# Optimization experiments

Hardware: AMD Instinct MI355X
Metric: run time of the kernel (lower is better)

The kernel has to match this reference:

```python
import jax, jax.numpy as jnp
import numpy as np

B = 16384    # batch of game states
HAND = 8     # max_hand_size
A = 30       # max_actions
C = 4        # max cards per action combo
E = 32       # card_embed_dim
HID = 128    # hidden_dim


def _encode_cards(cards, val_emb, suit_emb, type_emb):
    # cards: int array, 0 = padding, 53 = joker (treated as padding for value/suit)
    invalid = (cards == 0) | (cards == 53)
    values = jnp.where(invalid, 0, (cards - 1) % 13 + 1)
    suits = jnp.where(invalid, 0, (cards - 1) // 13 + 1)
    ce = jnp.concatenate([val_emb[values], suit_emb[suits]], axis=-1)  # [..., E]
    ct = jnp.where(values == 11, 1, jnp.where(values == 12, 2, jnp.where(values == 13, 3, 0)))
    te = type_emb[ct]  # [..., 8]
    pad = jnp.zeros(te.shape[:-1] + (E - te.shape[-1],), ce.dtype)
    return ce + jnp.concatenate([te, pad], axis=-1)


def _mha(q, kv, wq, bq, wk, bk, wv, bv, wo, bo, nh, kpm=None):
    b, sq, e = q.shape
    sk = kv.shape[1]
    hd = e // nh
    Q = (q @ wq + bq).reshape(b, sq, nh, hd)
    K = (kv @ wk + bk).reshape(b, sk, nh, hd)
    V = (kv @ wv + bv).reshape(b, sk, nh, hd)
    s = jnp.einsum('bqhd,bkhd->bhqk', Q, K) * (1.0 / np.sqrt(hd))
    if kpm is not None:  # kpm True = valid key
        s = s + jnp.where(kpm[:, None, None, :], 0.0, -1e9)
    a = jax.nn.softmax(s, axis=-1)
    o = jnp.einsum('bhqk,bkhd->bqhd', a, V).reshape(b, sq, e)
    return o @ wo + bo


def _combo_features(cards):
    # cards: [A, C] int, 0 = padding. Vectorized version of _compute_combo_features.
    mask = cards != 0
    combo_size = mask.sum(1).astype(jnp.float32)
    values = jnp.where(mask, (cards - 1) % 13 + 1, 0)
    has_valid = mask.any(1)
    fidx = jnp.argmax(mask, axis=1)
    fv = values[jnp.arange(cards.shape[0]), fidx]  # first valid value per action
    same = jnp.where(mask, values == fv[:, None], True).all(1).astype(jnp.float32)
    vf = values.astype(jnp.float32)
    attack = jnp.where(values == 1, 1.0,
             jnp.where(values == 11, 10.0,
             jnp.where(values == 12, 15.0,
             jnp.where(values == 13, 20.0, vf))))
    total = (attack * mask).sum(1)
    suits = jnp.where(mask, (cards - 1) // 13 + 1, 0)
    uniq = jnp.stack([(suits == s).any(1) for s in (1, 2, 3, 4)], 0).sum(0).astype(jnp.float32)
    ace = ((values == 1) & mask).any(1).astype(jnp.float32)
    valid = ((combo_size <= 4.0) & ((same > 0) | (ace > 0))).astype(jnp.float32)
    feats = jnp.stack([combo_size, same, total, uniq, ace, valid], axis=1)  # [A, 6]
    return jnp.where(has_valid[:, None], feats, 0.0), has_valid


def _forward(hand_cards, enemy_card, hand_size, game_state, discard_pile_cards,
             action_card_indices, num_valid_actions,
             val_emb, suit_emb, type_emb,
             ce_w1, ce_b1, ce_w2, ce_b2,
             ha_wq, ha_bq, ha_wk, ha_bk, ha_wv, ha_bv, ha_wo, ha_bo,
             he_wq, he_bq, he_wk, he_bk, he_wv, he_bv, he_wo, he_bo,
             se_w1, se_b1, se_w2, se_b2,
             atc_w1, atc_b1, atc_w2, atc_b2,
             as_w1, as_b1, as_w2, as_b2, as_w3, as_b3,
             cx_w1, cx_b1, cx_w2, cx_b2, cx_w3, cx_b3):
    relu = jax.nn.relu
    hand_emb = _encode_cards(hand_cards, val_emb, suit_emb, type_emb)            # [B, HAND, E]
    enemy_emb = _encode_cards(enemy_card[:, None], val_emb, suit_emb, type_emb)  # [B, 1, E]
    hand_mask = hand_cards != 0
    attended = _mha(hand_emb, hand_emb, ha_wq, ha_bq, ha_wk, ha_bk, ha_wv, ha_bv, ha_wo, ha_bo, 8, kpm=hand_mask)
    ctx_he = _mha(attended, enemy_emb, he_wq, he_bq, he_wk, he_bk, he_wv, he_bv, he_wo, he_bo, 4)
    lengths = jnp.maximum(hand_size.astype(jnp.float32), 1.0)[:, None]
    hand_ctx = ctx_he.sum(1) / lengths                                           # [B, E]

    # strategic features (batched per game state)
    hvals = jnp.where(hand_cards == 0, 0, (hand_cards - 1) % 13 + 1)
    hsz = hand_size.astype(jnp.float32)
    aces = (hvals == 1).sum(1).astype(jnp.float32)
    faces = ((hvals >= 11) & (hvals <= 13)).sum(1).astype(jnp.float32)
    low = ((hvals >= 2) & (hvals <= 6)).sum(1).astype(jnp.float32)
    hsuits = jnp.where(hand_cards == 0, 0, (hand_cards - 1) // 13 + 1)
    scnt = [(hsuits == s).sum(1).astype(jnp.float32) for s in (1, 2, 3, 4)]
    hvr = faces / (hsz + 1e-8)
    sdiv = jnp.stack([(hsuits == s).any(1) for s in (1, 2, 3, 4)], 0).sum(0).astype(jnp.float32) / 4.0
    strat = jnp.stack([hsz, aces, faces, low, scnt[0], scnt[1], scnt[2], scnt[3], hvr, sdiv], axis=1)
    strat_in = jnp.concatenate([game_state, strat], axis=1)                      # [B, 20]
    strat_ctx = relu(strat_in @ se_w1 + se_b1) @ se_w2 + se_b2                   # [B, 32]

    combined = jnp.concatenate([hand_ctx, enemy_emb[:, 0], strat_ctx, discard_pile_cards], axis=1)  # [B, 150]
    h = relu(combined @ cx_w1 + cx_b1)
    h = relu(h @ cx_w2 + cx_b2)
    ctx = h @ cx_w3 + cx_b3                                                      # [B, HID]
    type_probs = jax.nn.softmax(relu(ctx @ atc_w1 + atc_b1) @ atc_w2 + atc_b2, axis=-1)  # [B, 4]

    feats, has_valid = _combo_features(action_card_indices)                      # [A, 6], [A]
    emb = _encode_cards(action_card_indices, val_emb, suit_emb, type_emb)        # [A, C, E]
    m = (action_card_indices != 0).astype(emb.dtype)[..., None]
    cnt = jnp.maximum(m.sum(1), 1.0)
    act_emb = (emb * m).sum(1) / cnt                                             # masked mean over real cards
    act_emb = jnp.where(has_valid[:, None], act_emb, 0.0)
    combo_enc = relu(feats @ ce_w1 + ce_b1) @ ce_w2 + ce_b2                      # [A, 16]

    Bn = ctx.shape[0]
    af = jnp.concatenate([
        jnp.broadcast_to(ctx[:, None, :], (Bn, A, HID)),
        jnp.broadcast_to(act_emb[None], (Bn, A, E)),
        jnp.broadcast_to(combo_enc[None], (Bn, A, 16)),
    ], axis=-1)                                                                  # [B, A, 176]
    s = relu(af @ as_w1 + as_b1)
    s = relu(s @ as_w2 + as_b2)
    score = (s @ as_w3 + as_b3)[..., 0]                                          # [B, A]

    strength = feats[:, 2] / 20.0                                                # [A]
    bonus_valid = type_probs[:, 0:1] * strength[None, :] + type_probs[:, 1:2] * (1.0 - strength[None, :])
    bonus_empty = jnp.broadcast_to(type_probs[:, 3:4] * 2.0, (Bn, A))
    bonus = jnp.where(has_valid[None, :], bonus_valid, bonus_empty)
    return score + bonus                                                          # [B, A]


def setup_inputs() -> dict:
    key = jax.random.key(0)
    ki = iter(jax.random.split(key, 64))
    def nrm(shape, s):
        return (s * jax.random.normal(next(ki), shape)).astype(jnp.float32)
    def lin(i, o, s=0.08):
        return nrm((i, o), s), nrm((o,), 0.02)
    d = {}
    hc = jax.random.randint(next(ki), (B, HAND), 0, 53)
    d['hand_cards'] = hc.at[:, 0].set(jax.random.randint(next(ki), (B,), 1, 53))  # at least one valid card per hand
    d['enemy_card'] = jax.random.randint(next(ki), (B,), 1, 53)
    d['hand_size'] = jax.random.randint(next(ki), (B,), 1, 9)
    d['game_state'] = nrm((B, 10), 1.0)
    d['discard_pile_cards'] = jax.random.uniform(next(ki), (B, 54), dtype=jnp.float32)
    d['action_card_indices'] = jax.random.randint(next(ki), (A, C), 1, 53)
    d['num_valid_actions'] = A
    d['val_emb'] = nrm((14, 16), 0.1).at[0].set(0.0)   # padding_idx=0
    d['suit_emb'] = nrm((5, 16), 0.1).at[0].set(0.0)   # padding_idx=0
    d['type_emb'] = nrm((4, 8), 0.1)
    d['ce_w1'], d['ce_b1'] = lin(6, 32)
    d['ce_w2'], d['ce_b2'] = lin(32, 16)
    for p in ('ha', 'he'):
        for t in ('q', 'k', 'v', 'o'):
            d[p + '_w' + t], d[p + '_b' + t] = lin(E, E)
    d['se_w1'], d['se_b1'] = lin(20, 64)
    d['se_w2'], d['se_b2'] = lin(64, 32)
    d['atc_w1'], d['atc_b1'] = lin(HID, 64)
    d['atc_w2'], d['atc_b2'] = lin(64, 4)
    d['as_w1'], d['as_b1'] = lin(HID + E + 16, 64)
    d['as_w2'], d['as_b2'] = lin(64, 32)
    d['as_w3'], d['as_b3'] = lin(32, 1)
    d['cx_w1'], d['cx_b1'] = lin(2 * E + 32 + 54, HID)
    d['cx_w2'], d['cx_b2'] = lin(HID, HID)
    d['cx_w3'], d['cx_b3'] = lin(HID, HID)
    return d


def reference(hand_cards, enemy_card, hand_size, game_state, discard_pile_cards,
              action_card_indices, num_valid_actions,
              val_emb, suit_emb, type_emb,
              ce_w1, ce_b1, ce_w2, ce_b2,
              ha_wq, ha_bq, ha_wk, ha_bk, ha_wv, ha_bv, ha_wo, ha_bo,
              he_wq, he_bq, he_wk, he_bk, he_wv, he_bv, he_wo, he_bo,
              se_w1, se_b1, se_w2, se_b2,
              atc_w1, atc_b1, atc_w2, atc_b2,
              as_w1, as_b1, as_w2, as_b2, as_w3, as_b3,
              cx_w1, cx_b1, cx_w2, cx_b2, cx_w3, cx_b3):
    return _forward(hand_cards, enemy_card, hand_size, game_state, discard_pile_cards,
                    action_card_indices, num_valid_actions,
                    val_emb, suit_emb, type_emb,
                    ce_w1, ce_b1, ce_w2, ce_b2,
                    ha_wq, ha_bq, ha_wk, ha_bk, ha_wv, ha_bv, ha_wo, ha_bo,
                    he_wq, he_bq, he_wk, he_bk, he_wv, he_bv, he_wo, he_bo,
                    se_w1, se_b1, se_w2, se_b2,
                    atc_w1, atc_b1, atc_w2, atc_b2,
                    as_w1, as_b1, as_w2, as_b2, as_w3, as_b3,
                    cx_w1, cx_b1, cx_w2, cx_b2, cx_w3, cx_b3)
```

## Files before the change

kernel.cpp:

```cpp
#include <hip/hip_runtime.h>
#include <math.h>


__device__ __forceinline__ void encode_card32(int c,
                                              const float* __restrict__ val_emb,
                                              const float* __restrict__ suit_emb,
                                              const float* __restrict__ type_emb,
                                              float* e) {
  bool inv = (c == 0) || (c == 53);
  int v = inv ? 0 : ((c - 1) % 13 + 1);
  int s = inv ? 0 : ((c - 1) / 13 + 1);
  int ct = (v == 11) ? 1 : (v == 12) ? 2 : (v == 13) ? 3 : 0;
#pragma unroll
  for (int i = 0; i < 16; ++i) e[i] = val_emb[v * 16 + i];
#pragma unroll
  for (int i = 0; i < 16; ++i) e[16 + i] = suit_emb[s * 16 + i];
#pragma unroll
  for (int i = 0; i < 8; ++i) e[i] += type_emb[ct * 8 + i];
}

__global__ __launch_bounds__(256) void precompute_kernel(
    const int* __restrict__ acards,
    const float* __restrict__ val_emb, const float* __restrict__ suit_emb,
    const float* __restrict__ type_emb,
    const float* __restrict__ ce_w1, const float* __restrict__ ce_b1,
    const float* __restrict__ ce_w2, const float* __restrict__ ce_b2,
    const float* __restrict__ as_w1, const float* __restrict__ as_b1,
    const float* __restrict__ cx_w3, const float* __restrict__ cx_b3,
    const float* __restrict__ atc_w1, const float* __restrict__ atc_b1,
    float* __restrict__ ws) {
  const int tid = threadIdx.x;
  const int bid = blockIdx.x;

  if (bid > 0) {
    const int idx = (bid - 1) * 256 + tid;
    const int k = idx >> 6, j = idx & 63;
    float at = 0.f, ap = 0.f;
#pragma unroll 8
    for (int m = 0; m < 128; ++m) {
      float c = cx_w3[k * 128 + m];
      at += c * atc_w1[m * 64 + j];
      ap += c * as_w1[(size_t)m * 64 + j];
    }
    ws[2048 + idx] = at;
    ws[10304 + idx] = ap;
    return;
  }

  __shared__ float sAct[30][32];
  __shared__ float sCombo[30][16];

  if (tid >= 64 && tid < 128) {
    const int j = tid - 64;
    float bt = atc_b1[j], bp = 0.f;
#pragma unroll 8
    for (int m = 0; m < 128; ++m) {
      float c = cx_b3[m];
      bt += c * atc_w1[m * 64 + j];
      bp += c * as_w1[(size_t)m * 64 + j];
    }
    ws[10240 + j] = bt;
    ws[18496 + j] = bp;
  }

  if (tid < 30) {
    int c[4];
#pragma unroll
    for (int i = 0; i < 4; ++i) c[i] = acards[tid * 4 + i];
    bool mask[4]; int vals[4], suits[4]; int csize = 0; bool hasv = false;
#pragma unroll
    for (int i = 0; i < 4; ++i) {
      mask[i] = (c[i] != 0);
      if (mask[i]) { csize++; hasv = true; }
      vals[i] = mask[i] ? ((c[i] - 1) % 13 + 1) : 0;
      suits[i] = mask[i] ? ((c[i] - 1) / 13 + 1) : 0;
    }
    int fvv = mask[0] ? vals[0] : mask[1] ? vals[1] : mask[2] ? vals[2]
              : mask[3] ? vals[3] : vals[0];
    bool same = true;
#pragma unroll
    for (int i = 0; i < 4; ++i) if (mask[i] && vals[i] != fvv) same = false;
    float total = 0.f;
#pragma unroll
    for (int i = 0; i < 4; ++i) {
      if (mask[i]) {
        int v = vals[i];
        total += (v == 1) ? 1.f : (v == 11) ? 10.f : (v == 12) ? 15.f
                 : (v == 13) ? 20.f : (float)v;
      }
    }
    float uniq = 0.f;
#pragma unroll
    for (int s = 1; s <= 4; ++s) {
      bool any = false;
#pragma unroll
      for (int i = 0; i < 4; ++i) if (suits[i] == s) any = true;
      uniq += any ? 1.f : 0.f;
    }
    bool ace = false;
#pragma unroll
    for (int i = 0; i < 4; ++i) if (mask[i] && vals[i] == 1) ace = true;
    float f_same = same ? 1.f : 0.f, f_ace = ace ? 1.f : 0.f;
    float valid = (((float)csize <= 4.f) && (f_same > 0.f || f_ace > 0.f)) ? 1.f : 0.f;
    float feats[6] = {(float)csize, f_same, total, uniq, f_ace, valid};
    if (!hasv) { for (int i = 0; i < 6; ++i) feats[i] = 0.f; }
    float emb[32];
#pragma unroll
    for (int i = 0; i < 32; ++i) emb[i] = 0.f;
    float cnt = 0.f;
#pragma unroll
    for (int i = 0; i < 4; ++i) {
      float e[32];
      encode_card32(c[i], val_emb, suit_emb, type_emb, e);
      if (mask[i]) {
#pragma unroll
        for (int j = 0; j < 32; ++j) emb[j] += e[j];
        cnt += 1.f;
      }
    }
    float invc = 1.f / fmaxf(cnt, 1.f);
#pragma unroll
    for (int j = 0; j < 32; ++j) sAct[tid][j] = hasv ? emb[j] * invc : 0.f;
    float t32[32];
#pragma unroll
    for (int j = 0; j < 32; ++j) {
      float acc = ce_b1[j];
#pragma unroll
      for (int k = 0; k < 6; ++k) acc += feats[k] * ce_w1[k * 32 + j];
      t32[j] = fmaxf(acc, 0.f);
    }
#pragma unroll
    for (int j = 0; j < 16; ++j) {
      float acc = ce_b2[j];
#pragma unroll
      for (int k = 0; k < 32; ++k) acc += t32[k] * ce_w2[k * 16 + j];
      sCombo[tid][j] = acc;
    }
    ws[1920 + tid] = total * 0.05f;
    ws[1950 + tid] = hasv ? 1.f : 0.f;
  }
  __syncthreads();
  for (int idx = tid; idx < 1920; idx += 256) {
    int a = idx >> 6, j = idx & 63;
    float acc = as_b1[j];
#pragma unroll
    for (int k = 0; k < 32; ++k) acc += sAct[a][k] * as_w1[(128 + k) * 64 + j];
#pragma unroll
    for (int k = 0; k < 16; ++k) acc += sCombo[a][k] * as_w1[(160 + k) * 64 + j];
    ws[idx] = acc;
  }
}

template <int K, int NJ, bool RELU, bool HASB, bool QIN, bool QOUT>
__device__ __forceinline__ void layerU(
    const float* __restrict__ in, int inColBase, float* __restrict__ outB,
    int outColBase, const float* __restrict__ W, int ldw, int j0,
    const float* __restrict__ bias, int r) {
  float acc[NJ];
#pragma unroll
  for (int j = 0; j < NJ; ++j) acc[j] = HASB ? bias[j0 + j] : 0.f;
  if constexpr (QIN) {
    static_assert(K % 4 == 0, "quad input needs K%4==0");
    const int g0 = inColBase >> 2;
#pragma unroll 8
    for (int g = 0; g < K / 4; ++g) {
      float4 a = *(const float4*)&in[(g0 + g) * 256 + r * 4];
#pragma unroll
      for (int q = 0; q < 4; ++q) {
        float av = (q == 0) ? a.x : (q == 1) ? a.y : (q == 2) ? a.z : a.w;
        const float* wr = W + (size_t)(g * 4 + q) * ldw + j0;
#pragma unroll
        for (int j = 0; j < NJ; ++j) acc[j] += av * wr[j];
      }
    }
  } else {
#pragma unroll 4
    for (int k = 0; k < K; ++k) {
      float a = in[(inColBase + k) * 64 + r];
      const float* wr = W + (size_t)k * ldw + j0;
#pragma unroll
      for (int j = 0; j < NJ; ++j) acc[j] += a * wr[j];
    }
  }
#pragma unroll
  for (int j = 0; j < NJ; ++j) if (RELU) acc[j] = fmaxf(acc[j], 0.f);
  if constexpr (QOUT && (NJ % 4 == 0)) {
    const int c0 = outColBase + j0;
#pragma unroll
    for (int qg = 0; qg < NJ / 4; ++qg) {
      float4 o = make_float4(acc[qg * 4], acc[qg * 4 + 1],
                             acc[qg * 4 + 2], acc[qg * 4 + 3]);
      *(float4*)&outB[((c0 >> 2) + qg) * 256 + r * 4] = o;
    }
  } else {
#pragma unroll
    for (int j = 0; j < NJ; ++j) outB[(outColBase + j0 + j) * 64 + r] = acc[j];
  }
}

__global__ __launch_bounds__(1024) void policy_main(
    const int* __restrict__ hand_cards, const int* __restrict__ enemy_card,
    const int* __restrict__ hand_size, const float* __restrict__ game_state,
    const float* __restrict__ discard,
    const float* __restrict__ val_emb, const float* __restrict__ suit_emb,
    const float* __restrict__ type_emb,
    const float* __restrict__ he_wv, const float* __restrict__ he_bv,
    const float* __restrict__ he_wo, const float* __restrict__ he_bo,
    const float* __restrict__ se_w1, const float* __restrict__ se_b1,
    const float* __restrict__ se_w2, const float* __restrict__ se_b2,
    const float* __restrict__ atc_w2, const float* __restrict__ atc_b2,
    const float* __restrict__ as_w2, const float* __restrict__ as_b2,
    const float* __restrict__ as_w3, const float* __restrict__ as_b3,
    const float* __restrict__ cx_w1, const float* __restrict__ cx_b1,
    const float* __restrict__ cx_w2, const float* __restrict__ cx_b2,
    const float* __restrict__ ws, float* __restrict__ out) {
  __shared__ float bufA[38 * 256];
  __shared__ float bufB[128 * 64];

  const int tid = threadIdx.x;
  const int r = tid & 63;
  const int wq = __builtin_amdgcn_readfirstlane(tid >> 6);
  const int b0 = blockIdx.x * 64;

  for (int idx = tid; idx < 64 * 54; idx += 1024) {
    int rr = idx / 54, k = idx - rr * 54;
    int c = 96 + k;
    bufA[(c >> 2) * 256 + rr * 4 + (c & 3)] = discard[(size_t)b0 * 54 + idx];
  }
  if (wq == 2) {
#pragma unroll
    for (int k = 0; k < 10; ++k)
      bufB[k * 64 + r] = game_state[(size_t)(b0 + r) * 10 + k];
  }
  if (wq == 0) {
    const int b = b0 + r;
    const float hsz = (float)hand_size[b];
    int aces = 0, faces = 0, low = 0, c1 = 0, c2 = 0, c3 = 0, c4 = 0;
#pragma unroll
    for (int i = 0; i < 8; ++i) {
      int c = hand_cards[b * 8 + i];
      int v = (c == 0) ? 0 : ((c - 1) % 13 + 1);
      int s = (c == 0) ? 0 : ((c - 1) / 13 + 1);
      aces += (v == 1);
      faces += (v >= 11 && v <= 13);
      low += (v >= 2 && v <= 6);
      c1 += (s == 1); c2 += (s == 2); c3 += (s == 3); c4 += (s == 4);
    }
    float sdiv = (float)((c1 > 0) + (c2 > 0) + (c3 > 0) + (c4 > 0)) * 0.25f;
    float hvr = (float)faces / (hsz + 1e-8f);
    bufB[(10 + 0) * 64 + r] = hsz;          bufB[(10 + 1) * 64 + r] = (float)aces;
    bufB[(10 + 2) * 64 + r] = (float)faces; bufB[(10 + 3) * 64 + r] = (float)low;
    bufB[(10 + 4) * 64 + r] = (float)c1;    bufB[(10 + 5) * 64 + r] = (float)c2;
    bufB[(10 + 6) * 64 + r] = (float)c3;    bufB[(10 + 7) * 64 + r] = (float)c4;
    bufB[(10 + 8) * 64 + r] = hvr;          bufB[(10 + 9) * 64 + r] = sdiv;
  }
  if (wq == 1) {
    const int b = b0 + r;
    bufB[116 * 64 + r] = 8.0f / fmaxf((float)hand_size[b], 1.0f);
    float e[32];
    encode_card32(enemy_card[b], val_emb, suit_emb, type_emb, e);
#pragma unroll
    for (int g = 0; g < 8; ++g) {
      float4 ev = make_float4(e[g * 4], e[g * 4 + 1], e[g * 4 + 2], e[g * 4 + 3]);
      *(float4*)&bufA[(8 + g) * 256 + r * 4] = ev;
    }
  }
  __syncthreads();

  if (wq < 8) {
    layerU<20, 8, true, true, false, false>(bufB, 0, bufB, 20, se_w1, 64,
                                            wq * 8, se_b1, r);
  } else {
    layerU<32, 4, false, true, true, false>(bufA, 32, bufB, 84, he_wv, 32,
                                            (wq - 8) * 4, he_bv, r);
  }
  __syncthreads();

  if (wq < 8) {
    layerU<64, 4, false, true, false, true>(bufB, 20, bufA, 64, se_w2, 32,
                                            wq * 4, se_b2, r);
  } else {
    const int j0 = (wq - 8) * 4;
    float acc[4];
#pragma unroll
    for (int j = 0; j < 4; ++j) acc[j] = he_bo[j0 + j];
#pragma unroll 4
    for (int k = 0; k < 32; ++k) {
      float a = bufB[(84 + k) * 64 + r];
      const float* wr = he_wo + (size_t)k * 32 + j0;
#pragma unroll
      for (int j = 0; j < 4; ++j) acc[j] += a * wr[j];
    }
    float scale = bufB[116 * 64 + r];
    float4 o = make_float4(scale * acc[0], scale * acc[1],
                           scale * acc[2], scale * acc[3]);
    *(float4*)&bufA[(j0 >> 2) * 256 + r * 4] = o;
  }
  __syncthreads();

  {
    const int j0 = wq * 8;
    float acc[8];
#pragma unroll
    for (int j = 0; j < 8; ++j) acc[j] = cx_b1[j0 + j];
#pragma unroll 8
    for (int g = 0; g < 37; ++g) {
      float4 a = *(const float4*)&bufA[g * 256 + r * 4];
#pragma unroll
      for (int q = 0; q < 4; ++q) {
        float av = (q == 0) ? a.x : (q == 1) ? a.y : (q == 2) ? a.z : a.w;
        const float* wr = cx_w1 + (size_t)(g * 4 + q) * 128 + j0;
#pragma unroll
        for (int j = 0; j < 8; ++j) acc[j] += av * wr[j];
      }
    }
    {
      float4 a = *(const float4*)&bufA[37 * 256 + r * 4];
      const float* wr0 = cx_w1 + (size_t)148 * 128 + j0;
      const float* wr1 = cx_w1 + (size_t)149 * 128 + j0;
#pragma unroll
      for (int j = 0; j < 8; ++j) acc[j] += a.x * wr0[j] + a.y * wr1[j];
    }
#pragma unroll
    for (int qg = 0; qg < 2; ++qg) {
      float4 o = make_float4(fmaxf(acc[qg * 4], 0.f), fmaxf(acc[qg * 4 + 1], 0.f),
                             fmaxf(acc[qg * 4 + 2], 0.f), fmaxf(acc[qg * 4 + 3], 0.f));
      *(float4*)&bufB[((j0 >> 2) + qg) * 256 + r * 4] = o;
    }
  }
  __syncthreads();

  layerU<128, 8, true, true, true, true>(bufB, 0, bufA, 0, cx_w2, 128, wq * 8,
                                         cx_b2, r);
  __syncthreads();

  if (wq < 8) {
    layerU<128, 8, true, true, true, true>(bufA, 0, bufB, 0, ws + 2048, 64,
                                           wq * 8, ws + 10240, r);
  } else {
    layerU<128, 8, false, true, true, true>(bufA, 0, bufB, 64, ws + 10304, 64,
                                            (wq - 8) * 8, ws + 18496, r);
  }
  __syncthreads();

  if (wq < 15) {
    float lg0 = atc_b2[0], lg1 = atc_b2[1], lg2 = atc_b2[2], lg3 = atc_b2[3];
#pragma unroll 4
    for (int g = 0; g < 16; ++g) {
      float4 t = *(const float4*)&bufB[g * 256 + r * 4];
#pragma unroll
      for (int q = 0; q < 4; ++q) {
        float tv = (q == 0) ? t.x : (q == 1) ? t.y : (q == 2) ? t.z : t.w;
        const float* wr = atc_w2 + (size_t)(g * 4 + q) * 4;
        lg0 += tv * wr[0]; lg1 += tv * wr[1];
        lg2 += tv * wr[2]; lg3 += tv * wr[3];
      }
    }
    float m = fmaxf(fmaxf(lg0, lg1), fmaxf(lg2, lg3));
    float e0 = expf(lg0 - m), e1 = expf(lg1 - m), e2 = expf(lg2 - m), e3 = expf(lg3 - m);
    float inv = 1.f / (e0 + e1 + e2 + e3);
    float tp0 = e0 * inv, tp1 = e1 * inv, tp3 = e3 * inv;

    const float b3v = as_b3[0];
#pragma unroll 1
    for (int i = 0; i < 2; ++i) {
      const int a = wq * 2 + i;
      const float* qa = ws + a * 64;
      float acc[32];
#pragma unroll
      for (int j = 0; j < 32; ++j) acc[j] = 0.f;
#pragma unroll 4
      for (int g = 0; g < 16; ++g) {
        float4 pv = *(const float4*)&bufB[(16 + g) * 256 + r * 4];
#pragma unroll
        for (int q = 0; q < 4; ++q) {
          float p = (q == 0) ? pv.x : (q == 1) ? pv.y : (q == 2) ? pv.z : pv.w;
          const int k = g * 4 + q;
          float s = fmaxf(p + qa[k], 0.f);
          const float* w2r = as_w2 + (size_t)k * 32;
#pragma unroll
          for (int j = 0; j < 32; ++j) acc[j] += s * w2r[j];
        }
      }
      float sc = b3v;
#pragma unroll
      for (int j = 0; j < 32; ++j)
        sc += fmaxf(acc[j] + as_b2[j], 0.f) * as_w3[j];
      float st = ws[1920 + a], hv = ws[1950 + a];
      float bon = (hv > 0.5f) ? (tp0 * st + tp1 * (1.f - st)) : tp3 * 2.f;
      out[(size_t)(b0 + r) * 30 + a] = sc + bon;
    }
  }
}

extern "C" void kernel_launch(void* const* d_in, const int* in_sizes, int n_in,
                              void* d_out, int out_size, void* d_ws, size_t ws_size,
                              hipStream_t stream) {
  (void)in_sizes; (void)n_in; (void)out_size; (void)ws_size;
  const int* hand_cards = (const int*)d_in[0];
  const int* enemy_card = (const int*)d_in[1];
  const int* hand_size = (const int*)d_in[2];
  const float* game_state = (const float*)d_in[3];
  const float* discard = (const float*)d_in[4];
  const int* acards = (const int*)d_in[5];
  const float* val_emb = (const float*)d_in[7];
  const float* suit_emb = (const float*)d_in[8];
  const float* type_emb = (const float*)d_in[9];
  const float* ce_w1 = (const float*)d_in[10], * ce_b1 = (const float*)d_in[11];
  const float* ce_w2 = (const float*)d_in[12], * ce_b2 = (const float*)d_in[13];
  const float* he_wv = (const float*)d_in[26], * he_bv = (const float*)d_in[27];
  const float* he_wo = (const float*)d_in[28], * he_bo = (const float*)d_in[29];
  const float* se_w1 = (const float*)d_in[30], * se_b1 = (const float*)d_in[31];
  const float* se_w2 = (const float*)d_in[32], * se_b2 = (const float*)d_in[33];
  const float* atc_w1 = (const float*)d_in[34], * atc_b1 = (const float*)d_in[35];
  const float* atc_w2 = (const float*)d_in[36], * atc_b2 = (const float*)d_in[37];
  const float* as_w1 = (const float*)d_in[38], * as_b1 = (const float*)d_in[39];
  const float* as_w2 = (const float*)d_in[40], * as_b2 = (const float*)d_in[41];
  const float* as_w3 = (const float*)d_in[42], * as_b3 = (const float*)d_in[43];
  const float* cx_w1 = (const float*)d_in[44], * cx_b1 = (const float*)d_in[45];
  const float* cx_w2 = (const float*)d_in[46], * cx_b2 = (const float*)d_in[47];
  const float* cx_w3 = (const float*)d_in[48], * cx_b3 = (const float*)d_in[49];
  float* ws = (float*)d_ws;
  float* out = (float*)d_out;

  hipLaunchKernelGGL(precompute_kernel, dim3(33), dim3(256), 0, stream,
                     acards, val_emb, suit_emb, type_emb,
                     ce_w1, ce_b1, ce_w2, ce_b2, as_w1, as_b1,
                     cx_w3, cx_b3, atc_w1, atc_b1, ws);
  hipLaunchKernelGGL(policy_main, dim3(256), dim3(1024), 0, stream,
                     hand_cards, enemy_card, hand_size, game_state, discard,
                     val_emb, suit_emb, type_emb,
                     he_wv, he_bv, he_wo, he_bo,
                     se_w1, se_b1, se_w2, se_b2,
                     atc_w2, atc_b2,
                     as_w2, as_b2, as_w3, as_b3,
                     cx_w1, cx_b1, cx_w2, cx_b2,
                     ws, out);
}
```

Before: 244.0 us.

## Offload type-head softmax to idle wave and fuse two action-scorer loops

The 4-way type-prediction softmax was computed redundantly by each of the 15 working waves. It now runs once on the previously idle wave 15 and is shared through LDS after an extra barrier. The two per-wave action scorings are fused into one pass so each as_w2 weight load feeds two accumulators, and the two outputs are written as a single float2 store. This doubles the accumulator register count (64 floats), which may lower occupancy or cause spills.

```diff
diff --git a/kernel.cpp b/kernel.cpp
--- a/kernel.cpp
+++ b/kernel.cpp
@@ -343,7 +343,8 @@
   }
   __syncthreads();
 
-  if (wq < 15) {
+  float acc0[32], acc1[32];
+  if (wq == 15) {
     float lg0 = atc_b2[0], lg1 = atc_b2[1], lg2 = atc_b2[2], lg3 = atc_b2[3];
 #pragma unroll 4
     for (int g = 0; g < 16; ++g) {
@@ -359,37 +360,52 @@
     float m = fmaxf(fmaxf(lg0, lg1), fmaxf(lg2, lg3));
     float e0 = expf(lg0 - m), e1 = expf(lg1 - m), e2 = expf(lg2 - m), e3 = expf(lg3 - m);
     float inv = 1.f / (e0 + e1 + e2 + e3);
-    float tp0 = e0 * inv, tp1 = e1 * inv, tp3 = e3 * inv;
-
+    bufA[r]       = (e0 - e1) * inv;
+    bufA[64 + r]  = e1 * inv;
+    bufA[128 + r] = 2.f * e3 * inv;
+  } else {
+    const int a0 = wq * 2;
+    const float* qa = ws + a0 * 64;
+#pragma unroll
+    for (int j = 0; j < 32; ++j) { acc0[j] = 0.f; acc1[j] = 0.f; }
+#pragma unroll 4
+    for (int g = 0; g < 16; ++g) {
+      float4 pv = *(const float4*)&bufB[(16 + g) * 256 + r * 4];
+#pragma unroll
+      for (int q = 0; q < 4; ++q) {
+        float p = (q == 0) ? pv.x : (q == 1) ? pv.y : (q == 2) ? pv.z : pv.w;
+        const int k = g * 4 + q;
+        float s0 = fmaxf(p + qa[k], 0.f);
+        float s1 = fmaxf(p + qa[64 + k], 0.f);
+        const float* w2r = as_w2 + (size_t)k * 32;
+#pragma unroll
+        for (int j = 0; j < 32; ++j) {
+          float w = w2r[j];
+          acc0[j] += s0 * w;
+          acc1[j] += s1 * w;
+        }
+      }
+    }
+  }
+  __syncthreads();
+
+  if (wq < 15) {
+    const int a0 = wq * 2;
     const float b3v = as_b3[0];
-#pragma unroll 1
-    for (int i = 0; i < 2; ++i) {
-      const int a = wq * 2 + i;
-      const float* qa = ws + a * 64;
-      float acc[32];
-#pragma unroll
-      for (int j = 0; j < 32; ++j) acc[j] = 0.f;
-#pragma unroll 4
-      for (int g = 0; g < 16; ++g) {
-        float4 pv = *(const float4*)&bufB[(16 + g) * 256 + r * 4];
-#pragma unroll
-        for (int q = 0; q < 4; ++q) {
-          float p = (q == 0) ? pv.x : (q == 1) ? pv.y : (q == 2) ? pv.z : pv.w;
-          const int k = g * 4 + q;
-          float s = fmaxf(p + qa[k], 0.f);
-          const float* w2r = as_w2 + (size_t)k * 32;
-#pragma unroll
-          for (int j = 0; j < 32; ++j) acc[j] += s * w2r[j];
-        }
-      }
-      float sc = b3v;
-#pragma unroll
-      for (int j = 0; j < 32; ++j)
-        sc += fmaxf(acc[j] + as_b2[j], 0.f) * as_w3[j];
-      float st = ws[1920 + a], hv = ws[1950 + a];
-      float bon = (hv > 0.5f) ? (tp0 * st + tp1 * (1.f - st)) : tp3 * 2.f;
-      out[(size_t)(b0 + r) * 30 + a] = sc + bon;
-    }
+    float sc0 = b3v, sc1 = b3v;
+#pragma unroll
+    for (int j = 0; j < 32; ++j) {
+      float b2 = as_b2[j], w3 = as_w3[j];
+      sc0 += fmaxf(acc0[j] + b2, 0.f) * w3;
+      sc1 += fmaxf(acc1[j] + b2, 0.f) * w3;
+    }
+    float da = bufA[r], t1b = bufA[64 + r], t3x2 = bufA[128 + r];
+    float st0 = ws[1920 + a0], hv0 = ws[1950 + a0];
+    float st1 = ws[1921 + a0], hv1 = ws[1951 + a0];
+    float bon0 = (hv0 > 0.5f) ? (t1b + st0 * da) : t3x2;
+    float bon1 = (hv1 > 0.5f) ? (t1b + st1 * da) : t3x2;
+    *(float2*)&out[(size_t)(b0 + r) * 30 + a0] =
+        make_float2(sc0 + bon0, sc1 + bon1);
   }
 }
 
```

After: 222.7 us. 1.1x faster.
